# Kernel optimization log

Hardware: AMD Instinct MI355X
Metric: run time of the kernel (lower is better)

Reference implementation:

```python
import jax, jax.numpy as jnp
import numpy as np

NUM_HEADS = 16

def setup_inputs() -> dict:
    key = jax.random.key(0)
    ks = jax.random.split(key, 6)
    C = 512
    nW, B, N = 64, 4, 144
    x = jax.random.normal(ks[0], (B * nW, N, C), dtype=jnp.float32)
    mask = jax.random.randint(ks[1], (nW, N, N), 0, 2, dtype=jnp.int32)
    Wqkv = jax.random.normal(ks[2], (C, 3 * C), dtype=jnp.float32) * (1.0 / np.sqrt(C))
    bqkv = jnp.zeros((3 * C,), dtype=jnp.float32)
    Wproj = jax.random.normal(ks[3], (C, C), dtype=jnp.float32) * (1.0 / np.sqrt(C))
    bproj = jnp.zeros((C,), dtype=jnp.float32)
    return {"x": x, "mask": mask, "Wqkv": Wqkv, "bqkv": bqkv, "Wproj": Wproj, "bproj": bproj}

def reference(x, mask, Wqkv, bqkv, Wproj, bproj):
    Bn, N, C = x.shape
    H = NUM_HEADS
    D = C // H
    nW = mask.shape[0]
    B = Bn // nW
    scale = 1.0 / jnp.sqrt(jnp.asarray(D, dtype=x.dtype))

    qkv = x @ Wqkv + bqkv                        # (Bn, N, 3C)
    qkv = qkv.reshape(Bn, N, 3, H, D)            # packed order (qkv, H, D)
    qkv = jnp.transpose(qkv, (2, 0, 3, 1, 4))    # (3, Bn, H, N, D)
    q, k, v = qkv[0], qkv[1], qkv[2]

    # split window-batch dim: (B nW) -> B, nW
    q = q.reshape(B, nW, H, N, D)
    k = k.reshape(B, nW, H, N, D)
    v = v.reshape(B, nW, H, N, D)

    attn = jnp.einsum('bwhnd,bwhmd->bwhnm', q, k) * scale
    bias = jnp.where(mask == 0, -jnp.inf, 0.0).astype(x.dtype)  # (nW, N, N)
    attn = attn + bias.reshape(1, nW, 1, N, N)
    attn = jax.nn.softmax(attn, axis=-1)

    out = jnp.einsum('bwhnm,bwhmd->bwhnd', attn, v)   # (B, nW, H, N, D)
    out = jnp.transpose(out, (0, 1, 3, 2, 4)).reshape(Bn, N, C)
    return out @ Wproj + bproj
```

## Files before the change

kernel.cpp:

```cpp
#include <hip/hip_runtime.h>

typedef unsigned short u16;
typedef unsigned int u32;
typedef __attribute__((ext_vector_type(4))) float f32x4;
typedef __attribute__((ext_vector_type(8))) short bf16x8;
typedef __attribute__((ext_vector_type(4))) u32 u32x4;

__device__ __forceinline__ u16 f2bf(float f) {
  union { float f; u32 u; } v; v.f = f;
  u32 r = v.u + 0x7fffu + ((v.u >> 16) & 1u);
  return (u16)(r >> 16);
}

__device__ __forceinline__ void gload_lds16(const u16* g, u16* l) {
  __builtin_amdgcn_global_load_lds((__attribute__((address_space(1))) const void*)g,
                                   (__attribute__((address_space(3))) void*)l,
                                   16, 0, 0);
}

__global__ void __launch_bounds__(256) k_transpose_w(const float* __restrict__ W,
                                                     u16* __restrict__ Wt, int K, int Nc) {
  __shared__ u16 t[64][72];
  const int tid = threadIdx.x;
  const int kb = blockIdx.x * 64, nb = blockIdx.y * 64;
  const int c4 = (tid & 15) * 4;
  const int r0 = tid >> 4;
#pragma unroll
  for (int rr = 0; rr < 4; ++rr) {
    int r = rr * 16 + r0;
    float4 v = *(const float4*)(W + (size_t)(kb + r) * Nc + nb + c4);
    t[r][c4 + 0] = f2bf(v.x);
    t[r][c4 + 1] = f2bf(v.y);
    t[r][c4 + 2] = f2bf(v.z);
    t[r][c4 + 3] = f2bf(v.w);
  }
  __syncthreads();
  const int c8 = (tid & 7) * 8;
  const int rn = tid >> 3;
#pragma unroll
  for (int rr = 0; rr < 2; ++rr) {
    int n = rr * 32 + rn;
    u16 tmp[8];
#pragma unroll
    for (int j = 0; j < 8; ++j) tmp[j] = t[c8 + j][n];
    *(u32x4*)(Wt + (size_t)(nb + n) * K + kb + c8) = *(const u32x4*)tmp;
  }
}

__global__ void k_mask_bits(const int* __restrict__ mask, u32* __restrict__ mtab) {
  int idx = blockIdx.x * blockDim.x + threadIdx.x;
  if (idx >= 64 * 144 * 8) return;
  int wd = idx & 7;
  int r = idx >> 3;
  u32 bits = 0;
  if (wd < 5) {
    int base = r * 144 + wd * 32;
    int nmax = 144 - wd * 32;
    if (nmax > 32) nmax = 32;
    for (int b = 0; b < nmax; ++b) bits |= (mask[base + b] ? 1u : 0u) << b;
  }
  mtab[idx] = bits;
}

template <bool OUT_BF16, bool A_FP32>
__global__ void __launch_bounds__(256, 3) k_gemm(const void* __restrict__ Ap,
                                                 const u16* __restrict__ Bt,
                                                 const float* __restrict__ bias,
                                                 void* __restrict__ D,
                                                 int Nc, int K, int NB) {
  __shared__ u16 As[128 * 68];
  __shared__ u16 Bs[2][128 * 64];
  const int tid = threadIdx.x;
  const int wave = tid >> 6, lane = tid & 63;
  const int wr = wave >> 1, wc = wave & 1;
  const int l15 = lane & 15, g = lane >> 4;
  const int sx = l15 & 7;
  const f32x4 fzero = {0.f, 0.f, 0.f, 0.f};

  const int cpx = gridDim.x >> 3;
  const int swz = (blockIdx.x & 7) * cpx + (blockIdx.x >> 3);
  const int bm = swz / NB, bn = swz % NB;

  const u16* Bb = Bt + (size_t)bn * 128 * K;

  int rr[4], cc[4];
#pragma unroll
  for (int i = 0; i < 4; ++i) {
    int e = i * 256 + tid;
    rr[i] = e >> 3;
    cc[i] = e & 7;
  }

  f32x4 acc[4][4];
#pragma unroll
  for (int m = 0; m < 4; ++m)
#pragma unroll
    for (int n = 0; n < 4; ++n) acc[m][n] = fzero;

  f32x4 areg[8];
  u32x4 aregb[4];

  auto A_LOAD = [&](int ks) {
    if constexpr (A_FP32) {
      const float* Af = (const float*)Ap;
#pragma unroll
      for (int i = 0; i < 4; ++i) {
        const float* p = Af + (size_t)(bm * 128 + rr[i]) * K + ks + cc[i] * 8;
        areg[2 * i] = *(const f32x4*)(p);
        areg[2 * i + 1] = *(const f32x4*)(p + 4);
      }
    } else {
      const u16* Ab = (const u16*)Ap + (size_t)bm * 128 * K;
#pragma unroll
      for (int i = 0; i < 4; ++i)
        aregb[i] = *(const u32x4*)(Ab + (size_t)rr[i] * K + ks + cc[i] * 8);
    }
  };

  auto A_WRITE = [&]() {
#pragma unroll
    for (int i = 0; i < 4; ++i) {
      u32x4 wv;
      if constexpr (A_FP32) {
        u32 w0, w1, w2, w3;
        asm("v_cvt_pk_bf16_f32 %0, %1, %2" : "=v"(w0) : "v"(areg[2 * i][0]), "v"(areg[2 * i][1]));
        asm("v_cvt_pk_bf16_f32 %0, %1, %2" : "=v"(w1) : "v"(areg[2 * i][2]), "v"(areg[2 * i][3]));
        asm("v_cvt_pk_bf16_f32 %0, %1, %2" : "=v"(w2) : "v"(areg[2 * i + 1][0]), "v"(areg[2 * i + 1][1]));
        asm("v_cvt_pk_bf16_f32 %0, %1, %2" : "=v"(w3) : "v"(areg[2 * i + 1][2]), "v"(areg[2 * i + 1][3]));
        wv[0] = w0; wv[1] = w1; wv[2] = w2; wv[3] = w3;
      } else {
        wv = aregb[i];
      }
      *(u32x4*)(&As[rr[i] * 68 + cc[i] * 8]) = wv;
    }
  };

  auto B_STAGE = [&](int buf, int ks) {
#pragma unroll
    for (int i = 0; i < 4; ++i) {
      int cs = cc[i] ^ (rr[i] & 7);
      gload_lds16(Bb + (size_t)rr[i] * K + ks + (cs << 3), &Bs[buf][(i * 256 + tid) * 8]);
    }
  };

  auto COMPUTE = [&](int buf) {
#pragma unroll
    for (int kk = 0; kk < 2; ++kk) {
      bf16x8 a[4], b[4];
#pragma unroll
      for (int m = 0; m < 4; ++m)
        a[m] = *(const bf16x8*)(&As[(wr * 64 + m * 16 + l15) * 68 + (kk * 4 + g) * 8]);
#pragma unroll
      for (int n = 0; n < 4; ++n)
        b[n] = *(const bf16x8*)(&Bs[buf][(wc * 64 + n * 16 + l15) * 64 + (((kk * 4 + g) ^ sx) << 3)]);
#pragma unroll
      for (int m = 0; m < 4; ++m)
#pragma unroll
        for (int n = 0; n < 4; ++n)
          acc[m][n] = __builtin_amdgcn_mfma_f32_16x16x32_bf16(a[m], b[n], acc[m][n], 0, 0, 0);
    }
  };

  const int nt = K >> 6;
  A_LOAD(0);
  B_STAGE(0, 0);
  int cur = 0;
  for (int t = 0; t < nt; ++t) {
    asm volatile("s_waitcnt vmcnt(0)" ::: "memory");
    __builtin_amdgcn_sched_barrier(0);
    if (t + 1 < nt) B_STAGE(cur ^ 1, (t + 1) << 6);
    A_WRITE();
    if (t + 1 < nt) A_LOAD((t + 1) << 6);
    asm volatile("s_waitcnt lgkmcnt(0)" ::: "memory");
    __builtin_amdgcn_sched_barrier(0);
    __builtin_amdgcn_s_barrier();
    __builtin_amdgcn_sched_barrier(0);
    COMPUTE(cur);
    __builtin_amdgcn_sched_barrier(0);
    if (t + 1 < nt) __builtin_amdgcn_s_barrier();
    cur ^= 1;
  }

  const int row0 = bm * 128 + wr * 64;
  const int col0 = bn * 128 + wc * 64;
#pragma unroll
  for (int m = 0; m < 4; ++m) {
#pragma unroll
    for (int n = 0; n < 4; ++n) {
      int col = col0 + n * 16 + l15;
      float bv = bias[col];
#pragma unroll
      for (int j = 0; j < 4; ++j) {
        int row = row0 + m * 16 + g * 4 + j;
        float v = acc[m][n][j] + bv;
        if constexpr (OUT_BF16)
          ((u16*)D)[(size_t)row * Nc + col] = f2bf(v);
        else
          ((float*)D)[(size_t)row * Nc + col] = v;
      }
    }
  }
}

__global__ void __launch_bounds__(192) k_attn(const u16* __restrict__ qkv,
                                              const u32* __restrict__ mtab,
                                              u16* __restrict__ obuf) {
  __shared__ u16 k_s[144 * 40];
  __shared__ u16 vT_s[32 * 168];
  __shared__ u16 P_s[3][16 * 168];

  const int bh = blockIdx.x;
  const int bn = bh >> 4, h = bh & 15;
  const int wid = bn & 63;
  const int tid = threadIdx.x;
  const int wave = tid >> 6, lane = tid & 63;
  const int l15 = lane & 15, g = lane >> 4;
  const f32x4 fzero = {0.f, 0.f, 0.f, 0.f};

  const u16* base = qkv + (size_t)bn * 144 * 1536 + h * 32;

  for (int e = tid; e < 576; e += 192) {
    int n = e >> 2, c = e & 3;
    const u16* rowp = base + (size_t)n * 1536 + c * 8;
    u32x4 kv = *(const u32x4*)(rowp + 512);
    u32x4 vv = *(const u32x4*)(rowp + 1024);
    *(u32x4*)(k_s + n * 40 + c * 8) = kv;
#pragma unroll
    for (int t = 0; t < 4; ++t) {
      u32 w = vv[t];
      vT_s[(c * 8 + 2 * t) * 168 + n] = (u16)(w & 0xffffu);
      vT_s[(c * 8 + 2 * t + 1) * 168 + n] = (u16)(w >> 16);
    }
  }
  for (int e = tid; e < 512; e += 192) {
    int d = e >> 4, c = e & 15;
    vT_s[d * 168 + 144 + c] = 0;
  }
  __syncthreads();

  const float scale = 0.17677669529663687f;
  u16* Pw = &P_s[wave][0];

  for (int mt = wave; mt < 9; mt += 3) {
    bf16x8 qb = *(const bf16x8*)(base + (size_t)(mt * 16 + l15) * 1536 + g * 8);

    const u32* mp = mtab + ((size_t)(wid * 144 + mt * 16 + l15) << 3);
    u32 mw[5];
#pragma unroll
    for (int wd = 0; wd < 5; ++wd) mw[wd] = mp[wd];

    f32x4 accs[9];
#pragma unroll
    for (int nt = 0; nt < 9; ++nt) {
      bf16x8 kf = *(const bf16x8*)(k_s + (nt * 16 + l15) * 40 + g * 8);
      accs[nt] = __builtin_amdgcn_mfma_f32_16x16x32_bf16(kf, qb, fzero, 0, 0, 0);
    }

    float rmax = -1e30f;
#pragma unroll
    for (int nt = 0; nt < 9; ++nt) {
      const int wd = nt >> 1;
      const int shb = (nt & 1) * 16;
#pragma unroll
      for (int j = 0; j < 4; ++j) {
        float x = accs[nt][j] * scale;
        u32 bit = (mw[wd] >> (shb + g * 4 + j)) & 1u;
        x = bit ? x : -1e9f;
        accs[nt][j] = x;
        rmax = fmaxf(rmax, x);
      }
    }
    rmax = fmaxf(rmax, __shfl_xor(rmax, 16, 64));
    rmax = fmaxf(rmax, __shfl_xor(rmax, 32, 64));

    float rsum = 0.f;
#pragma unroll
    for (int nt = 0; nt < 9; ++nt)
#pragma unroll
      for (int j = 0; j < 4; ++j) {
        float p = __expf(accs[nt][j] - rmax);
        accs[nt][j] = p;
        rsum += p;
      }
    rsum += __shfl_xor(rsum, 16, 64);
    rsum += __shfl_xor(rsum, 32, 64);
    const float rinv = 1.f / rsum;

#pragma unroll
    for (int nt = 0; nt < 9; ++nt) {
      u32 w0, w1;
      float p0 = accs[nt][0] * rinv, p1 = accs[nt][1] * rinv;
      float p2 = accs[nt][2] * rinv, p3 = accs[nt][3] * rinv;
      asm("v_cvt_pk_bf16_f32 %0, %1, %2" : "=v"(w0) : "v"(p0), "v"(p1));
      asm("v_cvt_pk_bf16_f32 %0, %1, %2" : "=v"(w1) : "v"(p2), "v"(p3));
      *(u32*)(Pw + l15 * 168 + nt * 16 + g * 4) = w0;
      *(u32*)(Pw + l15 * 168 + nt * 16 + g * 4 + 2) = w1;
    }
    *(u32*)(Pw + l15 * 168 + 144 + g * 4) = 0;
    *(u32*)(Pw + l15 * 168 + 144 + g * 4 + 2) = 0;

    asm volatile("s_waitcnt lgkmcnt(0)" ::: "memory");
    __builtin_amdgcn_sched_barrier(0);

    f32x4 acco[2];
    acco[0] = fzero;
    acco[1] = fzero;
#pragma unroll
    for (int kk = 0; kk < 5; ++kk) {
      bf16x8 pa = *(const bf16x8*)(Pw + l15 * 168 + kk * 32 + g * 8);
#pragma unroll
      for (int nt2 = 0; nt2 < 2; ++nt2) {
        bf16x8 b = *(const bf16x8*)(vT_s + (nt2 * 16 + l15) * 168 + kk * 32 + g * 8);
        acco[nt2] = __builtin_amdgcn_mfma_f32_16x16x32_bf16(pa, b, acco[nt2], 0, 0, 0);
      }
    }
#pragma unroll
    for (int nt2 = 0; nt2 < 2; ++nt2)
#pragma unroll
      for (int j = 0; j < 4; ++j) {
        int r = mt * 16 + g * 4 + j;
        int d = nt2 * 16 + l15;
        obuf[((size_t)bn * 144 + r) * 512 + h * 32 + d] = f2bf(acco[nt2][j]);
      }
  }
}

extern "C" void kernel_launch(void* const* d_in, const int* in_sizes, int n_in,
                              void* d_out, int out_size, void* d_ws, size_t ws_size,
                              hipStream_t stream) {
  const float* x = (const float*)d_in[0];
  const int* mask = (const int*)d_in[1];
  const float* Wqkv = (const float*)d_in[2];
  const float* bqkv = (const float*)d_in[3];
  const float* Wproj = (const float*)d_in[4];
  const float* bproj = (const float*)d_in[5];
  float* out = (float*)d_out;

  char* ws = (char*)d_ws;
  u32* mtab    = (u32*)(ws + 0);
  u16* wqkv_t  = (u16*)(ws + 294912);
  u16* qkv     = (u16*)(ws + 1867776);
  u16* obuf    = (u16*)(ws + 115113984);
  u16* wproj_t = (u16*)(ws + 152862720);

  k_transpose_w<<<dim3(8, 24), 256, 0, stream>>>(Wqkv, wqkv_t, 512, 1536);
  k_transpose_w<<<dim3(8, 8), 256, 0, stream>>>(Wproj, wproj_t, 512, 512);
  k_mask_bits<<<288, 256, 0, stream>>>(mask, mtab);
  k_gemm<true, true><<<3456, 256, 0, stream>>>(x, wqkv_t, bqkv, qkv, 1536, 512, 12);
  k_attn<<<4096, 192, 0, stream>>>(qkv, mtab, obuf);
  k_gemm<false, false><<<1152, 256, 0, stream>>>(obuf, wproj_t, bproj, out, 512, 512, 4);
}
```

Measured before the change: 204.1 us.

## Prefetch A tiles two stages ahead with double register buffers in GEMM

The GEMM main loop now keeps two register buffers for the A operand and loads the tile two K-steps ahead. It waits with a partial vmcnt so that one A prefetch stays in flight while the current tile is written to LDS. Separately, the bf16 stores in the GEMM epilogue and the attention output now use the hardware cvt_pk_bf16 instruction instead of software rounding. This costs more registers, which may reduce occupancy, and the vmcnt(8) count must match the real number of outstanding loads (the A loads are issued after B_STAGE).

```diff
diff --git a/kernel.cpp b/kernel.cpp
--- a/kernel.cpp
+++ b/kernel.cpp
@@ -10,6 +10,12 @@
   union { float f; u32 u; } v; v.f = f;
   u32 r = v.u + 0x7fffu + ((v.u >> 16) & 1u);
   return (u16)(r >> 16);
+}
+
+__device__ __forceinline__ u16 f2bf_rne(float f) {
+  u32 w;
+  asm("v_cvt_pk_bf16_f32 %0, %1, %2" : "=v"(w) : "v"(f), "v"(f));
+  return (u16)w;
 }
 
 __device__ __forceinline__ void gload_lds16(const u16* g, u16* l) {
@@ -97,43 +103,42 @@
 #pragma unroll
     for (int n = 0; n < 4; ++n) acc[m][n] = fzero;
 
-  f32x4 areg[8];
-  u32x4 aregb[4];
-
-  auto A_LOAD = [&](int ks) {
-    if constexpr (A_FP32) {
-      const float* Af = (const float*)Ap;
-#pragma unroll
-      for (int i = 0; i < 4; ++i) {
-        const float* p = Af + (size_t)(bm * 128 + rr[i]) * K + ks + cc[i] * 8;
-        areg[2 * i] = *(const f32x4*)(p);
-        areg[2 * i + 1] = *(const f32x4*)(p + 4);
-      }
-    } else {
-      const u16* Ab = (const u16*)Ap + (size_t)bm * 128 * K;
-#pragma unroll
-      for (int i = 0; i < 4; ++i)
-        aregb[i] = *(const u32x4*)(Ab + (size_t)rr[i] * K + ks + cc[i] * 8);
-    }
-  };
-
-  auto A_WRITE = [&]() {
-#pragma unroll
-    for (int i = 0; i < 4; ++i) {
-      u32x4 wv;
-      if constexpr (A_FP32) {
-        u32 w0, w1, w2, w3;
-        asm("v_cvt_pk_bf16_f32 %0, %1, %2" : "=v"(w0) : "v"(areg[2 * i][0]), "v"(areg[2 * i][1]));
-        asm("v_cvt_pk_bf16_f32 %0, %1, %2" : "=v"(w1) : "v"(areg[2 * i][2]), "v"(areg[2 * i][3]));
-        asm("v_cvt_pk_bf16_f32 %0, %1, %2" : "=v"(w2) : "v"(areg[2 * i + 1][0]), "v"(areg[2 * i + 1][1]));
-        asm("v_cvt_pk_bf16_f32 %0, %1, %2" : "=v"(w3) : "v"(areg[2 * i + 1][2]), "v"(areg[2 * i + 1][3]));
-        wv[0] = w0; wv[1] = w1; wv[2] = w2; wv[3] = w3;
-      } else {
-        wv = aregb[i];
-      }
-      *(u32x4*)(&As[rr[i] * 68 + cc[i] * 8]) = wv;
-    }
-  };
+  f32x4 areg0[8], areg1[8];
+  u32x4 aregb0[4], aregb1[4];
+
+#define A_LOAD_M(AR, ARB, ks)                                                    \
+  {                                                                              \
+    if constexpr (A_FP32) {                                                      \
+      const float* Af = (const float*)Ap;                                        \
+      _Pragma("unroll") for (int i = 0; i < 4; ++i) {                            \
+        const float* p = Af + (size_t)(bm * 128 + rr[i]) * K + (ks) + cc[i] * 8; \
+        AR[2 * i] = *(const f32x4*)(p);                                          \
+        AR[2 * i + 1] = *(const f32x4*)(p + 4);                                  \
+      }                                                                          \
+    } else {                                                                     \
+      const u16* Ab = (const u16*)Ap + (size_t)bm * 128 * K;                     \
+      _Pragma("unroll") for (int i = 0; i < 4; ++i)                              \
+          ARB[i] = *(const u32x4*)(Ab + (size_t)rr[i] * K + (ks) + cc[i] * 8);   \
+    }                                                                            \
+  }
+
+#define A_WRITE_M(AR, ARB)                                                              \
+  {                                                                                     \
+    _Pragma("unroll") for (int i = 0; i < 4; ++i) {                                     \
+      u32x4 wv;                                                                         \
+      if constexpr (A_FP32) {                                                           \
+        u32 w0, w1, w2, w3;                                                             \
+        asm("v_cvt_pk_bf16_f32 %0, %1, %2" : "=v"(w0) : "v"(AR[2 * i][0]), "v"(AR[2 * i][1])); \
+        asm("v_cvt_pk_bf16_f32 %0, %1, %2" : "=v"(w1) : "v"(AR[2 * i][2]), "v"(AR[2 * i][3])); \
+        asm("v_cvt_pk_bf16_f32 %0, %1, %2" : "=v"(w2) : "v"(AR[2 * i + 1][0]), "v"(AR[2 * i + 1][1])); \
+        asm("v_cvt_pk_bf16_f32 %0, %1, %2" : "=v"(w3) : "v"(AR[2 * i + 1][2]), "v"(AR[2 * i + 1][3])); \
+        wv[0] = w0; wv[1] = w1; wv[2] = w2; wv[3] = w3;                                 \
+      } else {                                                                          \
+        wv = ARB[i];                                                                    \
+      }                                                                                 \
+      *(u32x4*)(&As[rr[i] * 68 + cc[i] * 8]) = wv;                                      \
+    }                                                                                   \
+  }
 
   auto B_STAGE = [&](int buf, int ks) {
 #pragma unroll
@@ -161,25 +166,40 @@
     }
   };
 
+#define GEMM_ITER(T, AW, AWB)                                                    \
+  {                                                                              \
+    const int t_ = (T);                                                          \
+    if (t_ + 1 < nt) {                                                           \
+      asm volatile("s_waitcnt vmcnt(8)" ::: "memory");                           \
+    } else {                                                                     \
+      asm volatile("s_waitcnt vmcnt(0)" ::: "memory");                           \
+    }                                                                            \
+    __builtin_amdgcn_sched_barrier(0);                                           \
+    if (t_ + 1 < nt) B_STAGE(cur ^ 1, (t_ + 1) << 6);                            \
+    A_WRITE_M(AW, AWB);                                                          \
+    if (t_ + 2 < nt) A_LOAD_M(AW, AWB, (t_ + 2) << 6);                           \
+    asm volatile("s_waitcnt lgkmcnt(0)" ::: "memory");                           \
+    __builtin_amdgcn_sched_barrier(0);                                           \
+    __builtin_amdgcn_s_barrier();                                                \
+    __builtin_amdgcn_sched_barrier(0);                                           \
+    COMPUTE(cur);                                                                \
+    __builtin_amdgcn_sched_barrier(0);                                           \
+    if (t_ + 1 < nt) __builtin_amdgcn_s_barrier();                               \
+    cur ^= 1;                                                                    \
+  }
+
   const int nt = K >> 6;
-  A_LOAD(0);
+  A_LOAD_M(areg0, aregb0, 0);
   B_STAGE(0, 0);
+  if (nt > 1) A_LOAD_M(areg1, aregb1, 64);
   int cur = 0;
-  for (int t = 0; t < nt; ++t) {
-    asm volatile("s_waitcnt vmcnt(0)" ::: "memory");
-    __builtin_amdgcn_sched_barrier(0);
-    if (t + 1 < nt) B_STAGE(cur ^ 1, (t + 1) << 6);
-    A_WRITE();
-    if (t + 1 < nt) A_LOAD((t + 1) << 6);
-    asm volatile("s_waitcnt lgkmcnt(0)" ::: "memory");
-    __builtin_amdgcn_sched_barrier(0);
-    __builtin_amdgcn_s_barrier();
-    __builtin_amdgcn_sched_barrier(0);
-    COMPUTE(cur);
-    __builtin_amdgcn_sched_barrier(0);
-    if (t + 1 < nt) __builtin_amdgcn_s_barrier();
-    cur ^= 1;
-  }
+  for (int tt = 0; tt < nt; tt += 2) {
+    GEMM_ITER(tt, areg0, aregb0);
+    if (tt + 1 < nt) GEMM_ITER(tt + 1, areg1, aregb1);
+  }
+#undef GEMM_ITER
+#undef A_WRITE_M
+#undef A_LOAD_M
 
   const int row0 = bm * 128 + wr * 64;
   const int col0 = bn * 128 + wc * 64;
@@ -194,7 +214,7 @@
         int row = row0 + m * 16 + g * 4 + j;
         float v = acc[m][n][j] + bv;
         if constexpr (OUT_BF16)
-          ((u16*)D)[(size_t)row * Nc + col] = f2bf(v);
+          ((u16*)D)[(size_t)row * Nc + col] = f2bf_rne(v);
         else
           ((float*)D)[(size_t)row * Nc + col] = v;
       }
@@ -320,7 +340,7 @@
       for (int j = 0; j < 4; ++j) {
         int r = mt * 16 + g * 4 + j;
         int d = nt2 * 16 + l15;
-        obuf[((size_t)bn * 144 + r) * 512 + h * 32 + d] = f2bf(acco[nt2][j]);
+        obuf[((size_t)bn * 144 + r) * 512 + h * 32 + d] = f2bf_rne(acco[nt2][j]);
       }
   }
 }
```

Result: slower. 335.1 us (+64.1%).
